# Kernel tuning notes

Hardware: AMD Instinct MI355X
Metric: run time of the kernel (lower is better)

## Reference

```python
import jax, jax.numpy as jnp
import numpy as np

N_NODES = 100000
HIDDEN = 64
N_REL = 9
N_LAYERS = 3
N_EDGES = 1000000


def setup_inputs() -> dict:
    key = jax.random.key(0)
    k1, k2, k3, k4, k5 = jax.random.split(key, 5)
    edge_index = jax.random.randint(k1, (2, N_EDGES), 0, N_NODES, dtype=jnp.int64)
    edge_type = jax.random.randint(k2, (N_EDGES,), 0, N_REL, dtype=jnp.int64)
    embeddings = jax.random.uniform(k3, (N_NODES, HIDDEN), dtype=jnp.float32)
    weights = jax.random.uniform(k4, (N_LAYERS, 2 * N_REL, HIDDEN, HIDDEN), dtype=jnp.float32)
    biases = jax.random.uniform(k5, (N_LAYERS, 2 * N_REL, HIDDEN), dtype=jnp.float32)
    return {"edge_index": edge_index, "edge_type": edge_type,
            "embeddings": embeddings, "weights": weights, "biases": biases}


def reference(edge_index, edge_type, embeddings, weights, biases):
    # Faithful translation of RGCNEncoder.forward.
    # NOTE (faithful to source): get_messages always reads self.embeddings,
    # and both `sources` and `dests` are edge_index[d][edge_type == r].
    N, E = embeddings.shape
    L = weights.shape[0]
    R = weights.shape[1] // 2
    idx0 = edge_index[0]          # indices for direction d=0 (source == dest)
    idx1 = edge_index[1]          # indices for direction d=1
    rel0 = edge_type              # weight row r + R*0
    rel1 = edge_type + R          # weight row r + R*1

    output = embeddings
    for l in range(L):
        # Transform every node under every (relation, direction) weight once,
        # then gather per edge. Equivalent to per-relation gather->matmul, but
        # avoids materializing per-edge [E,E] weight matrices.
        T = jnp.einsum('ne,reo->rno', embeddings, weights[l])   # [2R, N, E]
        m0 = T[rel0, idx0] + biases[l][rel0]                    # [n_edges, E]
        m1 = T[rel1, idx1] + biases[l][rel1]                    # [n_edges, E]
        m = jnp.concatenate([m0, m1], axis=0)
        d = jnp.concatenate([idx0, idx1], axis=0)
        # scatter_mean over destination nodes (0 for nodes with no messages)
        s = jax.ops.segment_sum(m, d, num_segments=N)
        cnt = jax.ops.segment_sum(jnp.ones((d.shape[0],), m.dtype), d, num_segments=N)
        hidden = jnp.where(cnt[:, None] > 0, s / jnp.maximum(cnt, 1.0)[:, None], 0.0)
        if l + 1 < L:
            hidden = jax.nn.relu(hidden)
        output = hidden
    return output
```

## Files before the change

### kernel.cpp

```cpp
#include <hip/hip_runtime.h>


typedef float  floatx4 __attribute__((ext_vector_type(4)));
typedef short  shortx8 __attribute__((ext_vector_type(8)));
typedef unsigned int uint;
typedef unsigned char uchar;

#define MFMA_BF16(A, B, C) __builtin_amdgcn_mfma_f32_16x16x32_bf16((A), (B), (C), 0, 0, 0)

#define NBUF 512
#define NBKT 512
#define CAP  48
#define PREPB 19

static __device__ __forceinline__ ushort f32_to_bf16_rne(float f) {
    union { float f; unsigned u; } v; v.f = f;
    unsigned r = v.u + 0x7fffu + ((v.u >> 16) & 1u);
    return (ushort)(r >> 16);
}

__global__ __launch_bounds__(256) void rgcn_scatter_prep(
    const int*   __restrict__ ei,
    const int*   __restrict__ et,
    const float* __restrict__ w2,
    const float* __restrict__ b2,
    ushort*      __restrict__ cnt_tab,
    ushort*      __restrict__ data,
    ushort*      __restrict__ wt_sw,
    ushort*      __restrict__ bias_sw,
    int E, int N)
{
    __shared__ uint   cur[NBKT];
    __shared__ ushort bins[NBKT][CAP];

    const int t = threadIdx.x;

    if (blockIdx.x >= NBUF) {
        int pb = blockIdx.x - NBUF;
        ushort* wlds = &bins[0][0];
        if (pb < 18) {
            const float* src = w2 + (pb << 12);
            #pragma unroll
            for (int i = 0; i < 16; i++) {
                int idx = t + 256 * i;
                wlds[idx] = f32_to_bf16_rne(src[idx]);
            }
            __syncthreads();
            ushort* dst = wt_sw + (pb << 12);
            #pragma unroll
            for (int u = 0; u < 16; u++) {
                int d = t * 16 + u;
                int cid  = d >> 9;
                int lane = (d >> 3) & 63;
                int j    = d & 7;
                int o = (cid >> 1) * 16 + (lane & 15);
                int k = (cid & 1) * 32 + (lane >> 4) * 8 + j;
                dst[d] = wlds[(k << 6) + o];
            }
        } else {
            #pragma unroll
            for (int u = 0; u < 8; u++) {
                int i2 = t * 8 + u;
                int nt   = i2 >> 9;
                int lane = (i2 >> 3) & 63;
                int j    = i2 & 7;
                int o  = nt * 16 + (lane & 15);
                int rr = (lane >> 4) * 8 + j;
                bias_sw[i2] = (rr < 18) ? f32_to_bf16_rne(b2[rr * 64 + o]) : (ushort)0;
            }
        }
        return;
    }

    #pragma unroll
    for (int b = t; b < NBKT; b += 256) cur[b] = 0;
    __syncthreads();

    const int epb = (E + NBUF - 1) / NBUF;
    const int e0 = blockIdx.x * epb;
    const int e1 = (e0 + epb < E) ? e0 + epb : E;

    for (int e = e0 + t; e < e1; e += 256) {
        int r = et[e]; int i0 = ei[e]; int i1 = ei[E + e];
        if ((unsigned)r < 9u) {
            if ((unsigned)i0 < (unsigned)N) {
                int b = i0 >> 8;
                uint o = atomicAdd(&cur[b], 1u);
                if (o < CAP) bins[b][o] = (ushort)((i0 & 255) * 18 + r);
            }
            if ((unsigned)i1 < (unsigned)N) {
                int b = i1 >> 8;
                uint o = atomicAdd(&cur[b], 1u);
                if (o < CAP) bins[b][o] = (ushort)((i1 & 255) * 18 + 9 + r);
            }
        }
    }
    __syncthreads();

    const int blk = blockIdx.x;
    for (int b = t; b < NBKT; b += 256) {
        uint c = cur[b];
        if (c > CAP) c = CAP;
        cnt_tab[(size_t)b * NBUF + blk] = (ushort)c;
        uint words = (c + 1) >> 1;
        uint* dst = (uint*)(data + ((size_t)b * NBUF + blk) * CAP);
        const uint* srcp = (const uint*)&bins[b][0];
        for (uint wd = 0; wd < words; wd++) dst[wd] = srcp[wd];
    }
}

__global__ void rgcn_prep_k(const float* __restrict__ w2, const float* __restrict__ b2,
                            ushort* __restrict__ wt_sw, ushort* __restrict__ bias_sw) {
    int i = blockIdx.x * 256 + threadIdx.x;
    const int WELEMS = 18 * 8 * 64 * 8;
    if (i < WELEMS) {
        int r    = i >> 12;
        int rem  = i & 4095;
        int cid  = rem >> 9;
        int lane = (rem >> 3) & 63;
        int j    = i & 7;
        int nt = cid >> 1, kh = cid & 1;
        int o = nt * 16 + (lane & 15);
        int k = kh * 32 + (lane >> 4) * 8 + j;
        wt_sw[i] = f32_to_bf16_rne(w2[(r << 12) + (k << 6) + o]);
    } else {
        int i2 = i - WELEMS;
        if (i2 < 2048) {
            int nt   = i2 >> 9;
            int lane = (i2 >> 3) & 63;
            int j    = i2 & 7;
            int o  = nt * 16 + (lane & 15);
            int rr = (lane >> 4) * 8 + j;
            bias_sw[i2] = (rr < 18) ? f32_to_bf16_rne(b2[rr * 64 + o]) : (ushort)0;
        }
    }
}
__global__ void rgcn_count32(const int* __restrict__ ei, const int* __restrict__ et,
                             int* __restrict__ cnts, int E, int N) {
    int e = blockIdx.x * 256 + threadIdx.x;
    if (e < E) {
        int r = et[e];
        int i0 = ei[e];
        int i1 = ei[E + e];
        if ((unsigned)r < 9u) {
            if ((unsigned)i0 < (unsigned)N) atomicAdd(&cnts[i0 * 18 + r], 1);
            if ((unsigned)i1 < (unsigned)N) atomicAdd(&cnts[i1 * 18 + 9 + r], 1);
        }
    }
}
__global__ void rgcn_cvt8(const int* __restrict__ c32, uchar* __restrict__ c8, int total4) {
    int i = blockIdx.x * 256 + threadIdx.x;
    if (i < total4) {
        uint v = 0;
        #pragma unroll
        for (int j = 0; j < 4; j++) {
            int c = c32[i * 4 + j];
            if (c > 255) c = 255;
            v |= ((uint)c) << (8 * j);
        }
        ((uint*)c8)[i] = v;
    }
}

static __device__ __forceinline__ void load_af(
    const float* __restrict__ emb, int n, int q, shortx8 af[2])
{
    const float* rp = emb + (size_t)n * 64 + q * 8;
    #pragma unroll
    for (int kh = 0; kh < 2; kh++) {
        floatx4 lo = *(const floatx4*)(rp + kh * 32);
        floatx4 hi = *(const floatx4*)(rp + kh * 32 + 4);
        shortx8 f;
        #pragma unroll
        for (int j = 0; j < 4; j++) {
            f[j]     = (short)f32_to_bf16_rne(lo[j]);
            f[j + 4] = (short)f32_to_bf16_rne(hi[j]);
        }
        af[kh] = f;
    }
}

static __device__ __forceinline__ void gemm_store(
    const shortx8 af[4][2],
    const float  (*__restrict__ wft)[256],
    const ushort (*__restrict__ wbL)[32],
    const ushort* __restrict__ wbase,
    const ushort* __restrict__ bias_sw,
    float* __restrict__ out, int N,
    int lrow, int rowbase, int m, int q, int lane)
{
    shortx8 bA[8], bB[8];
    #pragma unroll
    for (int c = 0; c < 8; c++) bA[c] = *(const shortx8*)(wbase + c * 512);

    floatx4 acc[4][4];
    #pragma unroll
    for (int mt = 0; mt < 4; mt++)
        #pragma unroll
        for (int nt = 0; nt < 4; nt++)
            acc[mt][nt] = (floatx4){0.f, 0.f, 0.f, 0.f};

    for (int r = 0; r < 18; r += 2) {
        __builtin_amdgcn_s_barrier();
        {
            const ushort* p = wbase + (size_t)(r + 1) * 4096;
            #pragma unroll
            for (int c = 0; c < 8; c++) bB[c] = *(const shortx8*)(p + c * 512);
        }
        {
            floatx4 swv[4];
            #pragma unroll
            for (int mt = 0; mt < 4; mt++)
                swv[mt] = *(const floatx4*)&wft[r][lrow + mt * 16 + q * 4];
            #pragma unroll
            for (int nt = 0; nt < 4; nt++)
                #pragma unroll
                for (int mt = 0; mt < 4; mt++) {
                    floatx4 tmp = (floatx4){0.f, 0.f, 0.f, 0.f};
                    tmp = MFMA_BF16(af[mt][0], bA[nt * 2 + 0], tmp);
                    tmp = MFMA_BF16(af[mt][1], bA[nt * 2 + 1], tmp);
                    acc[mt][nt] += swv[mt] * tmp;
                }
        }
        if (r + 2 < 18) {
            const ushort* p = wbase + (size_t)(r + 2) * 4096;
            #pragma unroll
            for (int c = 0; c < 8; c++) bA[c] = *(const shortx8*)(p + c * 512);
        }
        {
            floatx4 swv[4];
            #pragma unroll
            for (int mt = 0; mt < 4; mt++)
                swv[mt] = *(const floatx4*)&wft[r + 1][lrow + mt * 16 + q * 4];
            #pragma unroll
            for (int nt = 0; nt < 4; nt++)
                #pragma unroll
                for (int mt = 0; mt < 4; mt++) {
                    floatx4 tmp = (floatx4){0.f, 0.f, 0.f, 0.f};
                    tmp = MFMA_BF16(af[mt][0], bB[nt * 2 + 0], tmp);
                    tmp = MFMA_BF16(af[mt][1], bB[nt * 2 + 1], tmp);
                    acc[mt][nt] += swv[mt] * tmp;
                }
        }
    }

    #pragma unroll
    for (int nt = 0; nt < 4; nt++) {
        shortx8 btf = *(const shortx8*)(bias_sw + ((size_t)nt * 64 + lane) * 8);
        #pragma unroll
        for (int mt = 0; mt < 4; mt++) {
            shortx8 wfrag = *(const shortx8*)&wbL[lrow + mt * 16 + m][q * 8];
            acc[mt][nt] = MFMA_BF16(wfrag, btf, acc[mt][nt]);
        }
    }

    #pragma unroll
    for (int mt = 0; mt < 4; mt++)
        #pragma unroll
        for (int i = 0; i < 4; i++) {
            int nn = rowbase + mt * 16 + q * 4 + i;
            if (nn < N) {
                #pragma unroll
                for (int nt = 0; nt < 4; nt++)
                    out[(size_t)nn * 64 + nt * 16 + m] = acc[mt][nt][i];
            }
        }
}

__global__ __launch_bounds__(256, 2) void rgcn_main(
    const float*  __restrict__ emb,
    const ushort* __restrict__ cnt_tab,
    const ushort* __restrict__ data,
    const ushort* __restrict__ wt_sw,
    const ushort* __restrict__ bias_sw,
    float*        __restrict__ out,
    int N)
{
    __shared__ int    cnt[4608];
    __shared__ float  wft[18][256];
    __shared__ ushort wbL[256][32];
    __shared__ ushort scnt[NBUF];

    const int t    = threadIdx.x;
    const int b    = blockIdx.x;
    const int wave = t >> 6;
    const int lane = t & 63;
    const int m    = lane & 15;
    const int q    = lane >> 4;
    const int rowbase = b * 256 + wave * 64;
    const int lrow    = wave * 64;

    #pragma unroll
    for (int i = t; i < 4608; i += 256) cnt[i] = 0;
    #pragma unroll
    for (int w = t; w < NBUF; w += 256) scnt[w] = cnt_tab[(size_t)b * NBUF + w];

    shortx8 af[4][2];
    #pragma unroll
    for (int mt = 0; mt < 4; mt++) {
        int n = rowbase + mt * 16 + m;
        if (n >= N) n = N - 1;
        load_af(emb, n, q, af[mt]);
    }
    const ushort* wbase = wt_sw + (size_t)lane * 8;

    __syncthreads();

    #pragma unroll
    for (int w = t; w < NBUF; w += 256) {
        uint c = scnt[w];
        const ushort* seg = data + ((size_t)b * NBUF + w) * CAP;
        for (uint i = 0; i < c; i++) atomicAdd(&cnt[seg[i]], 1);
    }
    __syncthreads();

    {
        int c[18]; int s = 0;
        #pragma unroll
        for (int r = 0; r < 18; r++) { c[r] = cnt[t * 18 + r]; s += c[r]; }
        float inv = (s > 0) ? (1.0f / (float)s) : 0.0f;
        #pragma unroll
        for (int r = 0; r < 18; r++) {
            float w = (float)c[r] * inv;
            wft[r][t] = w;
            wbL[t][r] = f32_to_bf16_rne(w);
        }
        #pragma unroll
        for (int r = 18; r < 32; r++) wbL[t][r] = 0;
    }
    __syncthreads();

    gemm_store(af, wft, wbL, wbase, bias_sw, out, N, lrow, rowbase, m, q, lane);
}

__global__ __launch_bounds__(256, 2) void rgcn_main_c8(
    const float*  __restrict__ emb,
    const uchar*  __restrict__ cnts8,
    const ushort* __restrict__ wt_sw,
    const ushort* __restrict__ bias_sw,
    float*        __restrict__ out,
    int N)
{
    __shared__ float  wft[18][256];
    __shared__ ushort wbL[256][32];
    __shared__ uchar  craw[4608];

    const int t    = threadIdx.x;
    const int wave = t >> 6;
    const int lane = t & 63;
    const int m    = lane & 15;
    const int q    = lane >> 4;
    const int rowbase = blockIdx.x * 256 + wave * 64;
    const int lrow    = wave * 64;

    {
        const uint* srcp = (const uint*)(cnts8 + (size_t)blockIdx.x * 4608);
        uint* d = (uint*)craw;
        #pragma unroll
        for (int i = t; i < 1152; i += 256) d[i] = srcp[i];
    }
    shortx8 af[4][2];
    #pragma unroll
    for (int mt = 0; mt < 4; mt++) {
        int n = rowbase + mt * 16 + m;
        if (n >= N) n = N - 1;
        load_af(emb, n, q, af[mt]);
    }
    const ushort* wbase = wt_sw + (size_t)lane * 8;
    __syncthreads();
    {
        int c[18]; int s = 0;
        const uchar* cp = &craw[t * 18];
        #pragma unroll
        for (int r = 0; r < 18; r++) { c[r] = cp[r]; s += c[r]; }
        float inv = (s > 0) ? (1.0f / (float)s) : 0.0f;
        #pragma unroll
        for (int r = 0; r < 18; r++) {
            float w = (float)c[r] * inv;
            wft[r][t] = w;
            wbL[t][r] = f32_to_bf16_rne(w);
        }
        #pragma unroll
        for (int r = 18; r < 32; r++) wbL[t][r] = 0;
    }
    __syncthreads();
    gemm_store(af, wft, wbL, wbase, bias_sw, out, N, lrow, rowbase, m, q, lane);
}

extern "C" void kernel_launch(void* const* d_in, const int* in_sizes, int n_in,
                              void* d_out, int out_size, void* d_ws, size_t ws_size,
                              hipStream_t stream) {
    const int*   edge_index = (const int*)d_in[0];
    const int*   edge_type  = (const int*)d_in[1];
    const float* emb        = (const float*)d_in[2];
    const float* weights    = (const float*)d_in[3];
    const float* biases     = (const float*)d_in[4];
    float* out = (float*)d_out;

    const int E = in_sizes[1];
    const int N = in_sizes[2] / 64;
    const int nbuckets = (N + 255) >> 8;

    const float* w2 = weights + 2 * 18 * 64 * 64;
    const float* b2 = biases  + 2 * 18 * 64;

    size_t off = 0;
    auto take = [&](size_t bytes) { void* p = (char*)d_ws + off; off = (off + bytes + 63) & ~(size_t)63; return p; };
    ushort* cnt_tab = (ushort*)take((size_t)NBKT * NBUF * 2);
    ushort* data    = (ushort*)take((size_t)NBKT * NBUF * CAP * 2);
    ushort* wt_sw   = (ushort*)take(73728 * 2);
    ushort* bias_sw = (ushort*)take(2048 * 2);
    size_t need = off;

    if (ws_size >= need && nbuckets <= NBKT) {
        rgcn_scatter_prep<<<NBUF + PREPB, 256, 0, stream>>>(
            edge_index, edge_type, w2, b2, cnt_tab, data, wt_sw, bias_sw, E, N);
        rgcn_main<<<nbuckets, 256, 0, stream>>>(
            emb, cnt_tab, data, wt_sw, bias_sw, out, N);
    } else {
        int* c32 = (int*)d_ws;
        uchar* cnts8 = (uchar*)((char*)d_ws + (((size_t)nbuckets * 4608 * 4 + 63) & ~(size_t)63));
        wt_sw   = (ushort*)(cnts8 + (size_t)nbuckets * 4608);
        bias_sw = wt_sw + 73728;
        rgcn_prep_k<<<(73728 + 2048 + 255) / 256, 256, 0, stream>>>(w2, b2, wt_sw, bias_sw);
        hipMemsetAsync(c32, 0, (size_t)nbuckets * 4608 * 4, stream);
        rgcn_count32<<<(E + 255) / 256, 256, 0, stream>>>(edge_index, edge_type, c32, E, N);
        int total4 = nbuckets * 4608 / 4;
        rgcn_cvt8<<<(total4 + 255) / 256, 256, 0, stream>>>(c32, cnts8, total4);
        rgcn_main_c8<<<nbuckets, 256, 0, stream>>>(emb, cnts8, wt_sw, bias_sw, out, N);
    }
}
```

Before: 126.0 us.

## Stage edge bins in output buffer with inline counts and static weight globals

The per-bucket edge bins are now written into the output buffer itself, with each segment storing its count in its last slot, instead of separate workspace arrays and a count table. Swizzled weights and biases move to static device globals. The main kernel reads a bucket's own 64KB region before overwriting it with results, reads bins as packed 32-bit words, and bin capacity shrinks from 48 to 38. This removes the separate count-table load and packs the intermediate data more tightly. It risks dropping more edges on bucket overflow and depends on each block's staging region lying inside its own output rows.

```diff
diff --git a/kernel.cpp b/kernel.cpp
--- a/kernel.cpp
+++ b/kernel.cpp
@@ -10,8 +10,13 @@
 
 #define NBUF 512
 #define NBKT 512
-#define CAP  48
+#define CAP  38
+#define SEGW 40
+#define BROW 40
 #define PREPB 19
+
+__device__ ushort wt_g[73728];
+__device__ ushort bias_g[2048];
 
 static __device__ __forceinline__ ushort f32_to_bf16_rne(float f) {
     union { float f; unsigned u; } v; v.f = f;
@@ -24,14 +29,11 @@
     const int*   __restrict__ et,
     const float* __restrict__ w2,
     const float* __restrict__ b2,
-    ushort*      __restrict__ cnt_tab,
-    ushort*      __restrict__ data,
-    ushort*      __restrict__ wt_sw,
-    ushort*      __restrict__ bias_sw,
-    int E, int N)
+    float*       __restrict__ out,
+    int E, int N, int nbuckets)
 {
     __shared__ uint   cur[NBKT];
-    __shared__ ushort bins[NBKT][CAP];
+    __shared__ ushort bins[NBKT][BROW];
 
     const int t = threadIdx.x;
 
@@ -46,7 +48,7 @@
                 wlds[idx] = f32_to_bf16_rne(src[idx]);
             }
             __syncthreads();
-            ushort* dst = wt_sw + (pb << 12);
+            ushort* dst = wt_g + (pb << 12);
             #pragma unroll
             for (int u = 0; u < 16; u++) {
                 int d = t * 16 + u;
@@ -66,7 +68,7 @@
                 int j    = i2 & 7;
                 int o  = nt * 16 + (lane & 15);
                 int rr = (lane >> 4) * 8 + j;
-                bias_sw[i2] = (rr < 18) ? f32_to_bf16_rne(b2[rr * 64 + o]) : (ushort)0;
+                bias_g[i2] = (rr < 18) ? f32_to_bf16_rne(b2[rr * 64 + o]) : (ushort)0;
             }
         }
         return;
@@ -98,14 +100,15 @@
     __syncthreads();
 
     const int blk = blockIdx.x;
-    for (int b = t; b < NBKT; b += 256) {
+    for (int b = t; b < nbuckets; b += 256) {
         uint c = cur[b];
         if (c > CAP) c = CAP;
-        cnt_tab[(size_t)b * NBUF + blk] = (ushort)c;
+        ushort* seg = (ushort*)((char*)out + (size_t)b * 65536 + (size_t)blk * (SEGW * 2));
         uint words = (c + 1) >> 1;
-        uint* dst = (uint*)(data + ((size_t)b * NBUF + blk) * CAP);
+        uint* dst = (uint*)seg;
         const uint* srcp = (const uint*)&bins[b][0];
         for (uint wd = 0; wd < words; wd++) dst[wd] = srcp[wd];
+        seg[SEGW - 1] = (ushort)c;
     }
 }
 
@@ -185,7 +188,7 @@
     const float  (*__restrict__ wft)[256],
     const ushort (*__restrict__ wbL)[32],
     const ushort* __restrict__ wbase,
-    const ushort* __restrict__ bias_sw,
+    const ushort* __restrict__ bias_p,
     float* __restrict__ out, int N,
     int lrow, int rowbase, int m, int q, int lane)
 {
@@ -246,7 +249,7 @@
 
     #pragma unroll
     for (int nt = 0; nt < 4; nt++) {
-        shortx8 btf = *(const shortx8*)(bias_sw + ((size_t)nt * 64 + lane) * 8);
+        shortx8 btf = *(const shortx8*)(bias_p + ((size_t)nt * 64 + lane) * 8);
         #pragma unroll
         for (int mt = 0; mt < 4; mt++) {
             shortx8 wfrag = *(const shortx8*)&wbL[lrow + mt * 16 + m][q * 8];
@@ -269,17 +272,12 @@
 
 __global__ __launch_bounds__(256, 2) void rgcn_main(
     const float*  __restrict__ emb,
-    const ushort* __restrict__ cnt_tab,
-    const ushort* __restrict__ data,
-    const ushort* __restrict__ wt_sw,
-    const ushort* __restrict__ bias_sw,
-    float*        __restrict__ out,
+    float*        out,
     int N)
 {
     __shared__ int    cnt[4608];
     __shared__ float  wft[18][256];
     __shared__ ushort wbL[256][32];
-    __shared__ ushort scnt[NBUF];
 
     const int t    = threadIdx.x;
     const int b    = blockIdx.x;
@@ -292,8 +290,6 @@
 
     #pragma unroll
     for (int i = t; i < 4608; i += 256) cnt[i] = 0;
-    #pragma unroll
-    for (int w = t; w < NBUF; w += 256) scnt[w] = cnt_tab[(size_t)b * NBUF + w];
 
     shortx8 af[4][2];
     #pragma unroll
@@ -302,15 +298,22 @@
         if (n >= N) n = N - 1;
         load_af(emb, n, q, af[mt]);
     }
-    const ushort* wbase = wt_sw + (size_t)lane * 8;
-
-    __syncthreads();
-
+    const ushort* wbase = &wt_g[0] + (size_t)lane * 8;
+
+    __syncthreads();
+
+    const ushort* reg = (const ushort*)((const char*)out + (size_t)b * 65536);
     #pragma unroll
     for (int w = t; w < NBUF; w += 256) {
-        uint c = scnt[w];
-        const ushort* seg = data + ((size_t)b * NBUF + w) * CAP;
-        for (uint i = 0; i < c; i++) atomicAdd(&cnt[seg[i]], 1);
+        const ushort* seg = reg + w * SEGW;
+        uint c = seg[SEGW - 1];
+        const uint* sw = (const uint*)seg;
+        for (uint wd = 0; wd < (c >> 1); wd++) {
+            uint v = sw[wd];
+            atomicAdd(&cnt[v & 0xffffu], 1);
+            atomicAdd(&cnt[v >> 16], 1);
+        }
+        if (c & 1) atomicAdd(&cnt[seg[c - 1]], 1);
     }
     __syncthreads();
 
@@ -330,7 +333,7 @@
     }
     __syncthreads();
 
-    gemm_store(af, wft, wbL, wbase, bias_sw, out, N, lrow, rowbase, m, q, lane);
+    gemm_store(af, wft, wbL, wbase, &bias_g[0], out, N, lrow, rowbase, m, q, lane);
 }
 
 __global__ __launch_bounds__(256, 2) void rgcn_main_c8(
@@ -404,24 +407,20 @@
     const float* w2 = weights + 2 * 18 * 64 * 64;
     const float* b2 = biases  + 2 * 18 * 64;
 
-    size_t off = 0;
-    auto take = [&](size_t bytes) { void* p = (char*)d_ws + off; off = (off + bytes + 63) & ~(size_t)63; return p; };
-    ushort* cnt_tab = (ushort*)take((size_t)NBKT * NBUF * 2);
-    ushort* data    = (ushort*)take((size_t)NBKT * NBUF * CAP * 2);
-    ushort* wt_sw   = (ushort*)take(73728 * 2);
-    ushort* bias_sw = (ushort*)take(2048 * 2);
-    size_t need = off;
-
-    if (ws_size >= need && nbuckets <= NBKT) {
+    const int lastrows = N - 256 * (nbuckets - 1);
+    const bool fast = (nbuckets <= NBKT) &&
+                      ((size_t)lastrows * 256 >= (size_t)NBUF * (SEGW * 2)) &&
+                      ((size_t)out_size >= (size_t)N * 256);
+
+    if (fast) {
         rgcn_scatter_prep<<<NBUF + PREPB, 256, 0, stream>>>(
-            edge_index, edge_type, w2, b2, cnt_tab, data, wt_sw, bias_sw, E, N);
-        rgcn_main<<<nbuckets, 256, 0, stream>>>(
-            emb, cnt_tab, data, wt_sw, bias_sw, out, N);
+            edge_index, edge_type, w2, b2, out, E, N, nbuckets);
+        rgcn_main<<<nbuckets, 256, 0, stream>>>(emb, out, N);
     } else {
         int* c32 = (int*)d_ws;
         uchar* cnts8 = (uchar*)((char*)d_ws + (((size_t)nbuckets * 4608 * 4 + 63) & ~(size_t)63));
-        wt_sw   = (ushort*)(cnts8 + (size_t)nbuckets * 4608);
-        bias_sw = wt_sw + 73728;
+        ushort* wt_sw   = (ushort*)(cnts8 + (size_t)nbuckets * 4608);
+        ushort* bias_sw = wt_sw + 73728;
         rgcn_prep_k<<<(73728 + 2048 + 255) / 256, 256, 0, stream>>>(w2, b2, wt_sw, bias_sw);
         hipMemsetAsync(c32, 0, (size_t)nbuckets * 4608 * 4, stream);
         rgcn_count32<<<(E + 255) / 256, 256, 0, stream>>>(edge_index, edge_type, c32, E, N);
```

Result: slower. 190.9 us (+51.5%).
